# Kernel tuning notes

Measured on AMD Instinct MI355X. Metric: run time of the kernel, lower is better.

## Reference

```python
import jax, jax.numpy as jnp
import numpy as np

T, K, N, G = 8192, 1024, 2048, 8  # total_rows, k, n, num_groups


def setup_inputs() -> dict:
    key = jax.random.key(0)
    kA, kB, kO = jax.random.split(key, 3)
    A = jax.random.normal(kA, (T, K), dtype=jnp.float32)
    B = jax.random.normal(kB, (G, K, N), dtype=jnp.float32) * 0.02
    # monotonically increasing end-offsets; last offset covers all rows
    offsets = jnp.sort(jax.random.randint(kO, (G,), 1, T)).at[-1].set(T).astype(jnp.int32)
    return {"A": A, "B": B, "offsets": offsets}


def reference(A, B, offsets):
    """Grouped GEMM: rows A[offsets[g-1]:offsets[g]] are multiplied by B[g].

    Implemented jit-compatibly (offsets may be traced) by masking rows per
    group and accumulating disjoint contributions; the Python loop is over
    the small, static number of groups only.
    """
    num_groups = B.shape[0]
    total_rows = A.shape[0]
    # group id of each row: first offset strictly greater than row index
    gid = jnp.searchsorted(offsets, jnp.arange(total_rows), side="right")  # [T]
    out = jnp.zeros((total_rows, B.shape[2]), dtype=A.dtype)
    for g in range(num_groups):
        mask = (gid == g)[:, None]                      # [T,1] disjoint masks
        out = out + jnp.where(mask, A, 0.0) @ B[g]      # [T,n]
    return out
```

## Files before the change

kernel.cpp:

```cpp
#include <hip/hip_runtime.h>
#include <hip/hip_bf16.h>

#define T_ROWS 8192
#define K_DIM  1024
#define N_DIM  2048
#define G_NUM  8
#define CONVA_BLOCKS 2048
#define CONVB_BLOCKS 4096

typedef __attribute__((ext_vector_type(8))) short short8;
typedef __attribute__((ext_vector_type(4))) float v4f;

__device__ __forceinline__ unsigned short f2bf(float x) {
  unsigned int u = __builtin_bit_cast(unsigned int, x);
  u += 0x7fffu + ((u >> 16) & 1u);
  return (unsigned short)(u >> 16);
}
__device__ __forceinline__ unsigned int pk2(float a, float b) {
  return (unsigned int)f2bf(a) | ((unsigned int)f2bf(b) << 16);
}
__device__ __forceinline__ void async_cp16(const void* gsrc, void* ldst) {
  __builtin_amdgcn_global_load_lds(
      (const __attribute__((address_space(1))) void*)gsrc,
      (__attribute__((address_space(3))) void*)ldst, 16, 0, 0);
}

__global__ __launch_bounds__(256) void conv_fused(const float* __restrict__ A,
                                                  const float* __restrict__ B,
                                                  unsigned short* __restrict__ Ab,
                                                  unsigned short* __restrict__ Bt) {
  __shared__ float tile[64][65];
  const int bid = blockIdx.x;
  const int t = threadIdx.x;
  const int q3 = bid / 3, r3 = bid - q3 * 3;

  if (r3 == 0) {
    size_t idx = (size_t)q3 * 256 + t;
    const float4* src = (const float4*)A + idx * 4;
    float4 v0 = src[0], v1 = src[1], v2 = src[2], v3 = src[3];
    uint4 o0, o1;
    o0.x = pk2(v0.x, v0.y); o0.y = pk2(v0.z, v0.w);
    o0.z = pk2(v1.x, v1.y); o0.w = pk2(v1.z, v1.w);
    o1.x = pk2(v2.x, v2.y); o1.y = pk2(v2.z, v2.w);
    o1.z = pk2(v3.x, v3.y); o1.w = pk2(v3.z, v3.w);
    ((uint4*)Ab)[idx * 2]     = o0;
    ((uint4*)Ab)[idx * 2 + 1] = o1;
    return;
  }
  const int bidx = 2 * q3 + (r3 - 1);
  const int nt = bidx & 31;
  const int kt = (bidx >> 5) & 15;
  const int g  = bidx >> 9;
  const int c4 = t & 15;
  const int r  = t >> 4;

  const float* src = B + ((size_t)g * K_DIM + (size_t)kt * 64) * N_DIM + (size_t)nt * 64;
#pragma unroll
  for (int i = 0; i < 4; ++i) {
    int k = r + i * 16;
    float4 v = *(const float4*)(src + (size_t)k * N_DIM + c4 * 4);
    tile[k][c4 * 4 + 0] = v.x; tile[k][c4 * 4 + 1] = v.y;
    tile[k][c4 * 4 + 2] = v.z; tile[k][c4 * 4 + 3] = v.w;
  }
  __syncthreads();
  unsigned short* dst = Bt + ((size_t)g * N_DIM + (size_t)nt * 64) * K_DIM + (size_t)kt * 64;
#pragma unroll
  for (int i = 0; i < 2; ++i) {
    int idx = t + i * 256;
    int n = idx >> 3;
    int seg = idx & 7;
    unsigned int u0 = pk2(tile[seg * 8 + 0][n], tile[seg * 8 + 1][n]);
    unsigned int u1 = pk2(tile[seg * 8 + 2][n], tile[seg * 8 + 3][n]);
    unsigned int u2 = pk2(tile[seg * 8 + 4][n], tile[seg * 8 + 5][n]);
    unsigned int u3 = pk2(tile[seg * 8 + 6][n], tile[seg * 8 + 7][n]);
    uint4 o; o.x = u0; o.y = u1; o.z = u2; o.w = u3;
    *(uint4*)(dst + (size_t)n * K_DIM + seg * 8) = o;
  }
}

__global__ __launch_bounds__(256) void gemm_kernel(const unsigned short* __restrict__ Ab,
                                                   const unsigned short* __restrict__ Btb,
                                                   const int* __restrict__ offs,
                                                   float* __restrict__ out) {
  __shared__ unsigned short As[128 * 64];
  __shared__ unsigned short Bs[128 * 64];
  const int t = threadIdx.x;

  const int b = blockIdx.x;
  const int xcd = b & 7;
  const int j = b >> 3;
  const int mslot = xcd * 9 + (j >> 4);
  const int n0 = (j & 15) * 128;

  int prev = 0, cum = 0, row0 = 0, row_end = 0, g = 0, found = 0;
#pragma unroll
  for (int gg = 0; gg < G_NUM; ++gg) {
    int e = offs[gg];
    int tiles = (e - prev + 127) >> 7;
    if (!found && mslot < cum + tiles) {
      found = 1; g = gg; row0 = prev + (mslot - cum) * 128; row_end = e;
    }
    cum += tiles;
    prev = e;
  }
  if (!found) return;

  const int lane = t & 63;
  const int wv = t >> 6;
  const int wm = wv & 1;
  const int wn = wv >> 1;
  const int srcChunk = (t & 7) ^ ((t >> 3) & 7);

  const unsigned short* aSrc[4];
  const unsigned short* bSrc[4];
  char* aDst[4];
  char* bDst[4];
#pragma unroll
  for (int c = 0; c < 4; ++c) {
    int rl = c * 32 + (t >> 3);
    int rA = row0 + rl; if (rA > T_ROWS - 1) rA = T_ROWS - 1;
    aSrc[c] = Ab + (size_t)rA * K_DIM + srcChunk * 8;
    bSrc[c] = Btb + ((size_t)g * N_DIM + n0 + rl) * K_DIM + srcChunk * 8;
    aDst[c] = (char*)As + c * 4096 + t * 16;
    bDst[c] = (char*)Bs + c * 4096 + t * 16;
  }

  v4f acc[4][4];
#pragma unroll
  for (int i = 0; i < 4; ++i)
#pragma unroll
    for (int j2 = 0; j2 < 4; ++j2)
#pragma unroll
      for (int r = 0; r < 4; ++r) acc[i][j2][r] = 0.0f;

#pragma unroll
  for (int c = 0; c < 4; ++c) {
    async_cp16(aSrc[c], aDst[c]);
    async_cp16(bSrc[c], bDst[c]);
  }

  for (int k0 = 0; k0 < K_DIM; k0 += 64) {
    __syncthreads();
#pragma unroll
    for (int ks = 0; ks < 2; ++ks) {
      short8 a[4], bfr[4];
      int chBase = (lane >> 4) + ks * 4;
      int chPhys = chBase ^ (lane & 7);
#pragma unroll
      for (int im = 0; im < 4; ++im) {
        int row = wm * 64 + im * 16 + (lane & 15);
        a[im] = *(const short8*)((const char*)As + row * 128 + chPhys * 16);
      }
#pragma unroll
      for (int in = 0; in < 4; ++in) {
        int row = wn * 64 + in * 16 + (lane & 15);
        bfr[in] = *(const short8*)((const char*)Bs + row * 128 + chPhys * 16);
      }
#pragma unroll
      for (int im = 0; im < 4; ++im)
#pragma unroll
        for (int in = 0; in < 4; ++in)
          acc[im][in] = __builtin_amdgcn_mfma_f32_16x16x32_bf16(a[im], bfr[in], acc[im][in], 0, 0, 0);
    }
    if (k0 + 64 < K_DIM) {
      __syncthreads();
      int koff = k0 + 64;
#pragma unroll
      for (int c = 0; c < 4; ++c) {
        async_cp16(aSrc[c] + koff, aDst[c]);
        async_cp16(bSrc[c] + koff, bDst[c]);
      }
    }
  }

  const int colBase = n0 + wn * 64 + (lane & 15);
  const int rowBase = row0 + wm * 64 + ((lane >> 4) << 2);
#pragma unroll
  for (int im = 0; im < 4; ++im) {
#pragma unroll
    for (int in = 0; in < 4; ++in) {
      int c = colBase + in * 16;
#pragma unroll
      for (int r = 0; r < 4; ++r) {
        int rr = rowBase + im * 16 + r;
        if (rr < row_end) out[(size_t)rr * N_DIM + c] = acc[im][in][r];
      }
    }
  }
}

__global__ __launch_bounds__(256) void fallback_kernel(const float* __restrict__ A,
                                                       const float* __restrict__ B,
                                                       const int* __restrict__ offs,
                                                       float* __restrict__ out) {
  int r = blockIdx.y;
  int c = blockIdx.x * 256 + threadIdx.x;
  int g = 0;
#pragma unroll
  for (int i = 0; i < G_NUM; ++i) g += (offs[i] <= r);
  const float* a = A + (size_t)r * K_DIM;
  const float* b = B + (size_t)g * K_DIM * N_DIM + c;
  float s = 0.f;
  for (int k = 0; k < K_DIM; ++k) s += a[k] * b[(size_t)k * N_DIM];
  out[(size_t)r * N_DIM + c] = s;
}

extern "C" void kernel_launch(void* const* d_in, const int* in_sizes, int n_in,
                              void* d_out, int out_size, void* d_ws, size_t ws_size,
                              hipStream_t stream) {
  const float* A = (const float*)d_in[0];
  const float* B = (const float*)d_in[1];
  const int* offs = (const int*)d_in[2];
  float* out = (float*)d_out;

  size_t need = ((size_t)T_ROWS * K_DIM + (size_t)G_NUM * K_DIM * N_DIM) * 2;
  if (ws_size < need) {
    dim3 grid(N_DIM / 256, T_ROWS);
    fallback_kernel<<<grid, 256, 0, stream>>>(A, B, offs, out);
    return;
  }
  unsigned short* Ab = (unsigned short*)d_ws;
  unsigned short* Btb = Ab + (size_t)T_ROWS * K_DIM;

  conv_fused<<<CONVA_BLOCKS + CONVB_BLOCKS, 256, 0, stream>>>(A, B, Ab, Btb);
  gemm_kernel<<<8 * 9 * 16, 256, 0, stream>>>(Ab, Btb, offs, out);
}
```

Measured before the change: 185.4 us.

## Fuse A fp32-to-bf16 conversion into GEMM tile loading

Removes the A conversion from the prepass kernel and instead loads fp32 A directly in the GEMM, converting to bf16 in registers and storing into swizzled LDS. The next k-tile's A is prefetched into registers before the MFMA loop. This eliminates the bf16 A workspace write/read, but doubles A bytes fetched per GEMM tile and replaces async LDS copies with register-staged loads, raising register pressure.

Measured after the change: 309.9 us. 67.2% more time.

```diff
diff --git a/kernel.cpp b/kernel.cpp
--- a/kernel.cpp
+++ b/kernel.cpp
@@ -5,7 +5,6 @@
 #define K_DIM  1024
 #define N_DIM  2048
 #define G_NUM  8
-#define CONVA_BLOCKS 2048
 #define CONVB_BLOCKS 4096
 
 typedef __attribute__((ext_vector_type(8))) short short8;
@@ -25,29 +24,11 @@
       (__attribute__((address_space(3))) void*)ldst, 16, 0, 0);
 }
 
-__global__ __launch_bounds__(256) void conv_fused(const float* __restrict__ A,
-                                                  const float* __restrict__ B,
-                                                  unsigned short* __restrict__ Ab,
-                                                  unsigned short* __restrict__ Bt) {
+__global__ __launch_bounds__(256) void conv_b(const float* __restrict__ B,
+                                              unsigned short* __restrict__ Bt) {
   __shared__ float tile[64][65];
-  const int bid = blockIdx.x;
+  const int bidx = blockIdx.x;
   const int t = threadIdx.x;
-  const int q3 = bid / 3, r3 = bid - q3 * 3;
-
-  if (r3 == 0) {
-    size_t idx = (size_t)q3 * 256 + t;
-    const float4* src = (const float4*)A + idx * 4;
-    float4 v0 = src[0], v1 = src[1], v2 = src[2], v3 = src[3];
-    uint4 o0, o1;
-    o0.x = pk2(v0.x, v0.y); o0.y = pk2(v0.z, v0.w);
-    o0.z = pk2(v1.x, v1.y); o0.w = pk2(v1.z, v1.w);
-    o1.x = pk2(v2.x, v2.y); o1.y = pk2(v2.z, v2.w);
-    o1.z = pk2(v3.x, v3.y); o1.w = pk2(v3.z, v3.w);
-    ((uint4*)Ab)[idx * 2]     = o0;
-    ((uint4*)Ab)[idx * 2 + 1] = o1;
-    return;
-  }
-  const int bidx = 2 * q3 + (r3 - 1);
   const int nt = bidx & 31;
   const int kt = (bidx >> 5) & 15;
   const int g  = bidx >> 9;
@@ -78,7 +59,7 @@
   }
 }
 
-__global__ __launch_bounds__(256) void gemm_kernel(const unsigned short* __restrict__ Ab,
+__global__ __launch_bounds__(256) void gemm_kernel(const float* __restrict__ A,
                                                    const unsigned short* __restrict__ Btb,
                                                    const int* __restrict__ offs,
                                                    float* __restrict__ out) {
@@ -111,17 +92,17 @@
   const int wn = wv >> 1;
   const int srcChunk = (t & 7) ^ ((t >> 3) & 7);
 
-  const unsigned short* aSrc[4];
+  const float* aSrcF[4];
+  char* aDstW[4];
   const unsigned short* bSrc[4];
-  char* aDst[4];
   char* bDst[4];
 #pragma unroll
   for (int c = 0; c < 4; ++c) {
     int rl = c * 32 + (t >> 3);
     int rA = row0 + rl; if (rA > T_ROWS - 1) rA = T_ROWS - 1;
-    aSrc[c] = Ab + (size_t)rA * K_DIM + srcChunk * 8;
+    aSrcF[c] = A + (size_t)rA * K_DIM + (t & 7) * 8;
+    aDstW[c] = (char*)As + rl * 128 + srcChunk * 16;
     bSrc[c] = Btb + ((size_t)g * N_DIM + n0 + rl) * K_DIM + srcChunk * 8;
-    aDst[c] = (char*)As + c * 4096 + t * 16;
     bDst[c] = (char*)Bs + c * 4096 + t * 16;
   }
 
@@ -133,14 +114,35 @@
 #pragma unroll
       for (int r = 0; r < 4; ++r) acc[i][j2][r] = 0.0f;
 
-#pragma unroll
-  for (int c = 0; c < 4; ++c) {
-    async_cp16(aSrc[c], aDst[c]);
+  float4 af0[4], af1[4];
+#pragma unroll
+  for (int c = 0; c < 4; ++c) {
+    af0[c] = *(const float4*)(aSrcF[c]);
+    af1[c] = *(const float4*)(aSrcF[c] + 4);
+  }
+#pragma unroll
+  for (int c = 0; c < 4; ++c) {
     async_cp16(bSrc[c], bDst[c]);
+  }
+#pragma unroll
+  for (int c = 0; c < 4; ++c) {
+    uint4 o;
+    o.x = pk2(af0[c].x, af0[c].y); o.y = pk2(af0[c].z, af0[c].w);
+    o.z = pk2(af1[c].x, af1[c].y); o.w = pk2(af1[c].z, af1[c].w);
+    *(uint4*)aDstW[c] = o;
   }
 
   for (int k0 = 0; k0 < K_DIM; k0 += 64) {
     __syncthreads();
+    const bool more = (k0 + 64) < K_DIM;
+    if (more) {
+      int koff = k0 + 64;
+#pragma unroll
+      for (int c = 0; c < 4; ++c) {
+        af0[c] = *(const float4*)(aSrcF[c] + koff);
+        af1[c] = *(const float4*)(aSrcF[c] + koff + 4);
+      }
+    }
 #pragma unroll
     for (int ks = 0; ks < 2; ++ks) {
       short8 a[4], bfr[4];
@@ -162,12 +164,15 @@
         for (int in = 0; in < 4; ++in)
           acc[im][in] = __builtin_amdgcn_mfma_f32_16x16x32_bf16(a[im], bfr[in], acc[im][in], 0, 0, 0);
     }
-    if (k0 + 64 < K_DIM) {
+    if (more) {
       __syncthreads();
       int koff = k0 + 64;
 #pragma unroll
       for (int c = 0; c < 4; ++c) {
-        async_cp16(aSrc[c] + koff, aDst[c]);
+        uint4 o;
+        o.x = pk2(af0[c].x, af0[c].y); o.y = pk2(af0[c].z, af0[c].w);
+        o.z = pk2(af1[c].x, af1[c].y); o.w = pk2(af1[c].z, af1[c].w);
+        *(uint4*)aDstW[c] = o;
         async_cp16(bSrc[c] + koff, bDst[c]);
       }
     }
@@ -213,15 +218,14 @@
   const int* offs = (const int*)d_in[2];
   float* out = (float*)d_out;
 
-  size_t need = ((size_t)T_ROWS * K_DIM + (size_t)G_NUM * K_DIM * N_DIM) * 2;
+  size_t need = (size_t)G_NUM * K_DIM * N_DIM * 2;
   if (ws_size < need) {
     dim3 grid(N_DIM / 256, T_ROWS);
     fallback_kernel<<<grid, 256, 0, stream>>>(A, B, offs, out);
     return;
   }
-  unsigned short* Ab = (unsigned short*)d_ws;
-  unsigned short* Btb = Ab + (size_t)T_ROWS * K_DIM;
-
-  conv_fused<<<CONVA_BLOCKS + CONVB_BLOCKS, 256, 0, stream>>>(A, B, Ab, Btb);
-  gemm_kernel<<<8 * 9 * 16, 256, 0, stream>>>(Ab, Btb, offs, out);
-}
+  unsigned short* Btb = (unsigned short*)d_ws;
+
+  conv_b<<<CONVB_BLOCKS, 256, 0, stream>>>(B, Btb);
+  gemm_kernel<<<8 * 9 * 16, 256, 0, stream>>>(A, Btb, offs, out);
+}
```
